# Kernel tuning notes

Measured on AMD Instinct MI355X. Metric: run time of the kernel, lower is better.

The kernel has to match this reference:

```python
import jax, jax.numpy as jnp
import numpy as np

B, T, H, S, NH = 8, 4096, 1024, 64, 16
DH = H // NH
L = T // S  # tokens per sentence (contiguous partition)


def setup_inputs() -> dict:
    key = jax.random.key(0)
    ks = jax.random.split(key, 10)
    init = lambda k, shape: (jax.random.normal(k, shape, dtype=jnp.float32) * 0.02)
    starts = jnp.arange(S, dtype=jnp.int32) * L
    bounds = jnp.stack([starts, starts + L], axis=-1)  # [S,2]
    sentence_boundaries = jnp.broadcast_to(bounds, (B, S, 2))
    return {
        "context_hidden": jax.random.normal(ks[0], (B, T, H), dtype=jnp.float32),
        "sentence_boundaries": sentence_boundaries,
        "in_proj_w": init(ks[1], (3 * H, H)),
        "in_proj_b": jnp.zeros((3 * H,), jnp.float32),
        "out_w": init(ks[2], (H, H)),
        "out_b": jnp.zeros((H,), jnp.float32),
        "w1": init(ks[3], (H, 2 * H)),
        "b1": jnp.zeros((H,), jnp.float32),
        "w2": init(ks[4], (1, H)),
        "b2": jnp.zeros((1,), jnp.float32),
    }


def _forward(h, sentence_boundaries, in_proj_w, in_proj_b, out_w, out_b, w1, b1, w2, b2):
    starts = sentence_boundaries[:, :, 0]  # [B,S]
    ends = sentence_boundaries[:, :, 1]    # [B,S]
    t = jnp.arange(T, dtype=jnp.int32)
    # membership: token t belongs to sentence s iff start <= t < end
    member = (t[None, :, None] >= starts[:, None, :]) & (t[None, :, None] < ends[:, None, :])  # [B,T,S]
    mf = member.astype(h.dtype)
    counts = jnp.clip(mf.sum(axis=1), 1.0)  # [B,S]
    # segment mean pooling (encode_sentences)
    sent_repr = jnp.einsum('bts,bth->bsh', mf, h) / counts[..., None]  # [B,S,H]

    # multihead self-attention over sentence reprs (eval mode, no dropout)
    qkv = sent_repr @ in_proj_w.T + in_proj_b  # [B,S,3H]
    q, k, v = jnp.split(qkv, 3, axis=-1)
    q = q.reshape(B, S, NH, DH)
    k = k.reshape(B, S, NH, DH)
    v = v.reshape(B, S, NH, DH)
    scores = jnp.einsum('bqhd,bkhd->bhqk', q, k) / jnp.sqrt(jnp.asarray(DH, h.dtype))
    attn = jax.nn.softmax(scores, axis=-1)
    ctx = jnp.einsum('bhqk,bkhd->bqhd', attn, v).reshape(B, S, H)
    attended = ctx @ out_w.T + out_b  # [B,S,H]

    # gather each token's sentence repr
    sid = jnp.clip(member.astype(jnp.int32).argmax(axis=-1), 0, S - 1)  # [B,T]
    covered = member.any(axis=-1)  # [B,T]
    att_tok = jnp.take_along_axis(attended, sid[..., None], axis=1)  # [B,T,H]

    # coherence scorer MLP on concat([token, sent_repr]) without materializing concat
    hid = jax.nn.relu(h @ w1[:, :H].T + att_tok @ w1[:, H:].T + b1)  # [B,T,H]
    score = (hid @ w2.T + b2)[..., 0]  # [B,T]
    score = jnp.where(covered, score, 0.0)
    return h + score[..., None] * h


def reference(context_hidden, sentence_boundaries, in_proj_w, in_proj_b, out_w, out_b, w1, b1, w2, b2):
    return _forward(context_hidden, sentence_boundaries, in_proj_w, in_proj_b,
                    out_w, out_b, w1, b1, w2, b2)
```

## Files before the change

kernel.cpp:

```cpp
#include <hip/hip_runtime.h>
#include <stdint.h>

#define BB 8
#define TT 4096
#define HH 1024
#define SS 64
#define NHH 16
#define DHH 64

typedef __attribute__((ext_vector_type(8))) short short8;
typedef __attribute__((ext_vector_type(8))) unsigned short ushortx8;
typedef __attribute__((ext_vector_type(4))) float f32x4;
typedef unsigned short u16;

#define GLOAD16(gp, lp)                                                   \
  __builtin_amdgcn_global_load_lds(                                      \
      (const __attribute__((address_space(1))) void*)(gp),               \
      (__attribute__((address_space(3))) void*)(lp), 16, 0, 0)

__device__ __forceinline__ u16 f2bf(float f) {
  union { float f; uint32_t u; } v;
  v.f = f;
  uint32_t u = v.u;
  uint32_t r = u + 0x7fffu + ((u >> 16) & 1u);
  return (u16)(r >> 16);
}

__device__ __forceinline__ float bf2f(u16 b) {
  union { uint32_t u; float f; } v;
  v.u = ((uint32_t)b) << 16;
  return v.f;
}

__device__ __forceinline__ void stage_tile(u16* lds, const float* src, int ld, int tid) {
#pragma unroll
  for (int q = 0; q < 4; ++q) {
    int slot_id = tid + (q << 8);
    int row = slot_id >> 3;
    int sl = slot_id & 7;
    const float* p = src + (size_t)row * ld + (sl << 3);
    float4 x0 = *(const float4*)(p);
    float4 x1 = *(const float4*)(p + 4);
    ushortx8 o;
    o[0] = f2bf(x0.x); o[1] = f2bf(x0.y); o[2] = f2bf(x0.z); o[3] = f2bf(x0.w);
    o[4] = f2bf(x1.x); o[5] = f2bf(x1.y); o[6] = f2bf(x1.z); o[7] = f2bf(x1.w);
    *(ushortx8*)(&lds[(row << 6) + (((sl ^ (row & 7)) << 3))]) = o;
  }
}

__global__ __launch_bounds__(256) void conv_tile_kernel(const float* __restrict__ src,
                                                        int ld, int ntile_k,
                                                        u16* __restrict__ dst) {
  int bid = blockIdx.x;
  int rt = bid / ntile_k;
  int kt = bid - rt * ntile_k;
  const float* s0 = src + (size_t)rt * 128 * ld + kt * 64;
  u16* d0 = dst + (size_t)bid * 8192;
  int tid = threadIdx.x;
#pragma unroll
  for (int q = 0; q < 4; ++q) {
    int slot_id = tid + (q << 8);
    int row = slot_id >> 3;
    int sl = slot_id & 7;
    const float* p = s0 + (size_t)row * ld + (sl << 3);
    float4 x0 = *(const float4*)(p);
    float4 x1 = *(const float4*)(p + 4);
    ushortx8 o;
    o[0] = f2bf(x0.x); o[1] = f2bf(x0.y); o[2] = f2bf(x0.z); o[3] = f2bf(x0.w);
    o[4] = f2bf(x1.x); o[5] = f2bf(x1.y); o[6] = f2bf(x1.z); o[7] = f2bf(x1.w);
    *(ushortx8*)(&d0[(row << 6) + (((sl ^ (row & 7)) << 3))]) = o;
  }
}

__global__ __launch_bounds__(256) void pool_bf_kernel(const u16* __restrict__ hbf,
                                                      const int* __restrict__ bounds,
                                                      float* __restrict__ sent) {
  int bs = blockIdx.x;
  int b = bs >> 6;
  int start = bounds[bs * 2];
  int end = bounds[bs * 2 + 1];
  int lo = max(start, 0), hi = min(end, TT);
  int cnt = max(hi - lo, 0);
  float inv = 1.0f / (float)max(cnt, 1);
  int tid = threadIdx.x;
  int sg = tid >> 1;
  int half = tid & 1;
  int kt = sg >> 3, slot = sg & 7;
  float a[8] = {};
  for (int t = lo + half; t < hi; t += 2) {
    int grow = b * TT + t;
    int rt = grow >> 7, r = grow & 127;
    const u16* tile = hbf + ((size_t)rt * 16 + kt) * 8192;
    ushortx8 v = *(const ushortx8*)(&tile[(r << 6) + ((slot ^ (r & 7)) << 3)]);
#pragma unroll
    for (int j = 0; j < 8; ++j) a[j] += bf2f(v[j]);
  }
#pragma unroll
  for (int j = 0; j < 8; ++j) a[j] += __shfl_xor(a[j], 1);
  if (half == 0) {
    float* d = sent + (size_t)bs * HH + sg * 8;
#pragma unroll
    for (int j = 0; j < 8; ++j) d[j] = a[j] * inv;
  }
}

__global__ __launch_bounds__(256) void setup_misc(const float* __restrict__ ipb,
                                                  const float* __restrict__ outb,
                                                  const float* __restrict__ b1,
                                                  const int* __restrict__ bounds,
                                                  float* __restrict__ qkv,
                                                  float* __restrict__ att,
                                                  float* __restrict__ cbuf,
                                                  int* __restrict__ sid) {
  int idx = blockIdx.x * 256 + threadIdx.x;
  const int STR = 2048 * 256;
  for (int i = idx; i < 512 * 3072; i += STR) qkv[i] = ipb[i % 3072];
  for (int i = idx; i < 512 * 1024; i += STR) att[i] = outb[i & 1023];
  for (int i = idx; i < 512 * 1024; i += STR) cbuf[i] = b1[i & 1023];
  if (idx < BB * TT) {
    int b = idx >> 12, t = idx & (TT - 1);
    int r = -1;
    for (int s = 0; s < SS; ++s) {
      int st = bounds[(b * SS + s) * 2], en = bounds[(b * SS + s) * 2 + 1];
      if (t >= st && t < en) { r = s; break; }
    }
    sid[idx] = r;
  }
}

__global__ __launch_bounds__(256) void gemm_bt_atomic(const float* __restrict__ A, int lda,
                                                      const float* __restrict__ Bm, int ldb,
                                                      float* __restrict__ C, int ldc,
                                                      int kper) {
  __shared__ u16 As[128 * 64];
  __shared__ u16 Bs[128 * 64];
  int tid = threadIdx.x;
  int m0 = blockIdx.x * 128, n0 = blockIdx.y * 128;
  int kbeg = blockIdx.z * kper;
  f32x4 acc[4][4] = {};

  for (int k0 = kbeg; k0 < kbeg + kper; k0 += 64) {
    __syncthreads();
    stage_tile(As, A + (size_t)m0 * lda + k0, lda, tid);
    stage_tile(Bs, Bm + (size_t)n0 * ldb + k0, ldb, tid);
    __syncthreads();
    int lane = tid & 63, wid = tid >> 6;
    int wm = wid >> 1, wn = wid & 1;
    int lr = lane & 15, lg = lane >> 4;
#pragma unroll
    for (int kk = 0; kk < 2; ++kk) {
      short8 af[4], bfr[4];
#pragma unroll
      for (int i = 0; i < 4; ++i) {
        int arow = wm * 64 + i * 16 + lr;
        int aslot = (kk * 4 + lg) ^ (arow & 7);
        af[i] = *(const short8*)(&As[(arow << 6) + (aslot << 3)]);
        int brow = wn * 64 + i * 16 + lr;
        int bslot = (kk * 4 + lg) ^ (brow & 7);
        bfr[i] = *(const short8*)(&Bs[(brow << 6) + (bslot << 3)]);
      }
#pragma unroll
      for (int i = 0; i < 4; ++i)
#pragma unroll
        for (int j = 0; j < 4; ++j)
          acc[i][j] = __builtin_amdgcn_mfma_f32_16x16x32_bf16(af[i], bfr[j], acc[i][j], 0, 0, 0);
    }
  }

  int lane = tid & 63, wid = tid >> 6;
  int wm = wid >> 1, wn = wid & 1;
  int lr = lane & 15, lg = lane >> 4;
#pragma unroll
  for (int i = 0; i < 4; ++i)
#pragma unroll
    for (int j = 0; j < 4; ++j)
#pragma unroll
      for (int r = 0; r < 4; ++r) {
        int row = m0 + wm * 64 + i * 16 + lg * 4 + r;
        int col = n0 + wn * 64 + j * 16 + lr;
        atomicAdd(&C[(size_t)row * ldc + col], acc[i][j][r]);
      }
}

__global__ __launch_bounds__(256) void attn_kernel(const float* __restrict__ qkv,
                                                   float* __restrict__ ctx) {
  int bh = blockIdx.x;
  int b = bh >> 4, nh = bh & 15;
  __shared__ float q[64][64], k[64][64], v[64][64], s[64][64];
  int tid = threadIdx.x;
  const float* base = qkv + (size_t)b * SS * 3072 + nh * 64;
  for (int e = tid; e < 4096; e += 256) {
    int i = e >> 6, d = e & 63;
    q[i][d] = base[(size_t)i * 3072 + d];
    k[i][d] = base[(size_t)i * 3072 + 1024 + d];
    v[i][d] = base[(size_t)i * 3072 + 2048 + d];
  }
  __syncthreads();
  for (int e = tid; e < 4096; e += 256) {
    int i = e >> 6, j = e & 63;
    float acc = 0.f;
#pragma unroll 8
    for (int d = 0; d < 64; ++d) acc += q[i][d] * k[j][d];
    s[i][j] = acc * 0.125f;
  }
  __syncthreads();
  {
    int r = tid >> 2, sub = tid & 3;
    int j0 = sub * 16;
    float m = -1e30f;
#pragma unroll
    for (int j = 0; j < 16; ++j) m = fmaxf(m, s[r][j0 + j]);
    m = fmaxf(m, __shfl_xor(m, 1));
    m = fmaxf(m, __shfl_xor(m, 2));
    float sum = 0.f;
#pragma unroll
    for (int j = 0; j < 16; ++j) {
      float e_ = __expf(s[r][j0 + j] - m);
      s[r][j0 + j] = e_;
      sum += e_;
    }
    sum += __shfl_xor(sum, 1);
    sum += __shfl_xor(sum, 2);
    float inv = 1.0f / sum;
#pragma unroll
    for (int j = 0; j < 16; ++j) s[r][j0 + j] *= inv;
  }
  __syncthreads();
  for (int e = tid; e < 4096; e += 256) {
    int i = e >> 6, d = e & 63;
    float acc = 0.f;
#pragma unroll 8
    for (int j = 0; j < 64; ++j) acc += s[i][j] * v[j][d];
    ctx[((size_t)b * SS + i) * HH + nh * 64 + d] = acc;
  }
}

__global__ __launch_bounds__(512, 4) void score_partial(const u16* __restrict__ hbf,
                                                        const u16* __restrict__ wbf,
                                                        const float* __restrict__ cbuf,
                                                        const float* __restrict__ w2,
                                                        const int* __restrict__ sid_arr,
                                                        float* __restrict__ score_part) {
  __shared__ u16 As[8192];
  __shared__ u16 Bs[16384];
  __shared__ float w2_lds[256];
  __shared__ int sid_lds[128];
  __shared__ float red[128];

  int tid = threadIdx.x;
  int bid = blockIdx.x;
  int x = bid & 7;
  int g = bid >> 3;
  int mt = x * 32 + (g >> 2);
  int c = g & 3;
  int n0 = c * 256;
  size_t g0 = (size_t)mt * 128;
  int b = (int)(g0 >> 12);
  const u16* asrc = hbf + (size_t)mt * 16 * 8192;

  if (tid < 256) w2_lds[tid] = w2[n0 + tid];
  if (tid < 128) {
    sid_lds[tid] = sid_arr[g0 + tid];
    red[tid] = 0.f;
  }

  int lane = tid & 63, wid = tid >> 6;
  int wm = wid >> 2, wn = wid & 3;
  int lr = lane & 15, lg = lane >> 4;

  f32x4 acc[4][4] = {};
  for (int kt = 0; kt < 16; ++kt) {
    __syncthreads();
    const u16* at = asrc + kt * 8192;
#pragma unroll
    for (int q = 0; q < 2; ++q) {
      int off = q * 4096 + wid * 512;
      GLOAD16(at + off + lane * 8, &As[off]);
    }
#pragma unroll
    for (int q = 0; q < 4; ++q) {
      int half = q >> 1;
      int boff = (q & 1) * 4096 + wid * 512;
      const u16* bt = wbf + ((size_t)(2 * c + half) * 16 + kt) * 8192;
      GLOAD16(bt + boff + lane * 8, &Bs[half * 8192 + boff]);
    }
    __syncthreads();
#pragma unroll
    for (int kk = 0; kk < 2; ++kk) {
      short8 af[4], bfr[4];
#pragma unroll
      for (int i = 0; i < 4; ++i) {
        int arow = wm * 64 + i * 16 + lr;
        int aslot = (kk * 4 + lg) ^ (arow & 7);
        af[i] = *(const short8*)(&As[(arow << 6) + (aslot << 3)]);
      }
#pragma unroll
      for (int j = 0; j < 4; ++j) {
        int brow = wn * 64 + j * 16 + lr;
        int half = (wn * 64 + j * 16) >> 7;
        int r = brow & 127;
        int bslot = (kk * 4 + lg) ^ (r & 7);
        bfr[j] = *(const short8*)(&Bs[(half << 13) + (r << 6) + (bslot << 3)]);
      }
#pragma unroll
      for (int i = 0; i < 4; ++i)
#pragma unroll
        for (int j = 0; j < 4; ++j)
          acc[i][j] = __builtin_amdgcn_mfma_f32_16x16x32_bf16(af[i], bfr[j], acc[i][j], 0, 0, 0);
    }
  }

  float sp[4][4];
#pragma unroll
  for (int i = 0; i < 4; ++i) {
#pragma unroll
    for (int r = 0; r < 4; ++r) {
      int rowl = wm * 64 + i * 16 + lg * 4 + r;
      int s = sid_lds[rowl];
      int sc = s < 0 ? 0 : s;
      const float* crow = cbuf + ((size_t)b * SS + sc) * HH + n0;
      float accs = 0.f;
#pragma unroll
      for (int j = 0; j < 4; ++j) {
        int coll = wn * 64 + j * 16 + lr;
        float t = acc[i][j][r] + crow[coll];
        if (t > 0.f) accs += t * w2_lds[coll];
      }
      sp[i][r] = accs;
    }
  }

#pragma unroll
  for (int i = 0; i < 4; ++i)
#pragma unroll
    for (int r = 0; r < 4; ++r) {
      float v = sp[i][r];
      v += __shfl_xor(v, 1);
      v += __shfl_xor(v, 2);
      v += __shfl_xor(v, 4);
      v += __shfl_xor(v, 8);
      sp[i][r] = v;
    }
  if (lr == 0) {
#pragma unroll
    for (int i = 0; i < 4; ++i)
#pragma unroll
      for (int r = 0; r < 4; ++r)
        atomicAdd(&red[wm * 64 + i * 16 + lg * 4 + r], sp[i][r]);
  }
  __syncthreads();
  if (tid < 128) score_part[(size_t)c * (BB * TT) + g0 + tid] = red[tid];
}

__global__ __launch_bounds__(256) void scale_kernel(const u16* __restrict__ hbf,
                                                    const float* __restrict__ score_part,
                                                    const float* __restrict__ b2,
                                                    const int* __restrict__ sid_arr,
                                                    float* __restrict__ out) {
  __shared__ float fac[16];
  int tid = threadIdx.x;
  int r0 = blockIdx.x * 16;
  if (tid < 16) {
    int t = r0 + tid;
    float s = b2[0];
#pragma unroll
    for (int c = 0; c < 4; ++c) s += score_part[(size_t)c * (BB * TT) + t];
    fac[tid] = (sid_arr[t] >= 0) ? (1.0f + s) : 1.0f;
  }
  __syncthreads();
  for (int e = tid; e < 16 * 128; e += 256) {
    int row = e >> 7, grp = e & 127;
    int kt = grp >> 3, slot = grp & 7;
    int grow = r0 + row;
    int rt = grow >> 7, r = grow & 127;
    const u16* tile = hbf + ((size_t)rt * 16 + kt) * 8192;
    ushortx8 v = *(const ushortx8*)(&tile[(r << 6) + ((slot ^ (r & 7)) << 3)]);
    float f = fac[row];
    float4 o0, o1;
    o0.x = bf2f(v[0]) * f; o0.y = bf2f(v[1]) * f; o0.z = bf2f(v[2]) * f; o0.w = bf2f(v[3]) * f;
    o1.x = bf2f(v[4]) * f; o1.y = bf2f(v[5]) * f; o1.z = bf2f(v[6]) * f; o1.w = bf2f(v[7]) * f;
    float4* dst = (float4*)(out + (size_t)grow * HH + grp * 8);
    dst[0] = o0;
    dst[1] = o1;
  }
}

extern "C" void kernel_launch(void* const* d_in, const int* in_sizes, int n_in,
                              void* d_out, int out_size, void* d_ws, size_t ws_size,
                              hipStream_t stream) {
  const float* h        = (const float*)d_in[0];
  const int*   bounds   = (const int*)d_in[1];
  const float* in_proj_w = (const float*)d_in[2];
  const float* in_proj_b = (const float*)d_in[3];
  const float* out_w    = (const float*)d_in[4];
  const float* out_b    = (const float*)d_in[5];
  const float* w1       = (const float*)d_in[6];
  const float* b1       = (const float*)d_in[7];
  const float* w2       = (const float*)d_in[8];
  const float* b2       = (const float*)d_in[9];
  float* out = (float*)d_out;

  char* ws = (char*)d_ws;
  float* sent  = (float*)(ws);
  float* qkv   = (float*)(ws + (2ull << 20));
  float* ctx   = (float*)(ws + (8ull << 20));
  float* att   = (float*)(ws + (10ull << 20));
  float* cbuf  = (float*)(ws + (12ull << 20));
  int*   sid   = (int*)(ws + (14ull << 20));
  float* spart = (float*)(ws + (15ull << 20));
  u16*   hbf   = (u16*)(ws + (16ull << 20));
  u16*   wbf   = (u16*)(ws + (80ull << 20));

  conv_tile_kernel<<<256 * 16, 256, 0, stream>>>(h, HH, 16, hbf);
  conv_tile_kernel<<<8 * 16, 256, 0, stream>>>(w1, 2 * HH, 16, wbf);

  pool_bf_kernel<<<BB * SS, 256, 0, stream>>>(hbf, bounds, sent);
  setup_misc<<<2048, 256, 0, stream>>>(in_proj_b, out_b, b1, bounds, qkv, att, cbuf, sid);

  gemm_bt_atomic<<<dim3(4, 24, 4), 256, 0, stream>>>(sent, HH, in_proj_w, HH, qkv, 3 * HH, 256);
  attn_kernel<<<BB * NHH, 256, 0, stream>>>(qkv, ctx);
  gemm_bt_atomic<<<dim3(4, 8, 4), 256, 0, stream>>>(ctx, HH, out_w, HH, att, HH, 256);
  gemm_bt_atomic<<<dim3(4, 8, 4), 256, 0, stream>>>(att, HH, w1 + HH, 2 * HH, cbuf, HH, 256);

  score_partial<<<1024, 512, 0, stream>>>(hbf, wbf, cbuf, w2, sid, spart);
  scale_kernel<<<2048, 256, 0, stream>>>(hbf, spart, b2, sid, out);
}
```

Baseline: 288.7 us.

## Enlarge score GEMM tile to 256x256 with 1024-thread blocks; merge conversion launches

The token-scoring GEMM now uses 256x256 output tiles per block (16 waves, 1024 threads) instead of 128x256. Each loaded weight tile is reused across twice as many token rows, which cuts global/L2 traffic for W1 per output. The two fp32-to-bf16 conversion launches are also merged into one kernel to save a launch. The larger block halves the grid to 512 blocks and raises LDS use and per-CU register pressure, which may lower occupancy and latency hiding.

```diff
diff --git a/kernel.cpp b/kernel.cpp
--- a/kernel.cpp
+++ b/kernel.cpp
@@ -48,14 +48,19 @@
   }
 }
 
-__global__ __launch_bounds__(256) void conv_tile_kernel(const float* __restrict__ src,
-                                                        int ld, int ntile_k,
-                                                        u16* __restrict__ dst) {
+__global__ __launch_bounds__(256) void conv_both_kernel(const float* __restrict__ h,
+                                                        u16* __restrict__ hbf,
+                                                        const float* __restrict__ w1,
+                                                        u16* __restrict__ wbf) {
   int bid = blockIdx.x;
-  int rt = bid / ntile_k;
-  int kt = bid - rt * ntile_k;
+  const float* src;
+  int ld, tbid;
+  u16* dst;
+  if (bid < 4096) { src = h;  ld = 1024; dst = hbf; tbid = bid; }
+  else            { src = w1; ld = 2048; dst = wbf; tbid = bid - 4096; }
+  int rt = tbid >> 4, kt = tbid & 15;
   const float* s0 = src + (size_t)rt * 128 * ld + kt * 64;
-  u16* d0 = dst + (size_t)bid * 8192;
+  u16* d0 = dst + (size_t)tbid * 8192;
   int tid = threadIdx.x;
 #pragma unroll
   for (int q = 0; q < 4; ++q) {
@@ -235,54 +240,51 @@
   }
 }
 
-__global__ __launch_bounds__(512, 4) void score_partial(const u16* __restrict__ hbf,
-                                                        const u16* __restrict__ wbf,
-                                                        const float* __restrict__ cbuf,
-                                                        const float* __restrict__ w2,
-                                                        const int* __restrict__ sid_arr,
-                                                        float* __restrict__ score_part) {
-  __shared__ u16 As[8192];
-  __shared__ u16 Bs[16384];
+__global__ __launch_bounds__(1024, 4) void score_partial(const u16* __restrict__ hbf,
+                                                         const u16* __restrict__ wbf,
+                                                         const float* __restrict__ cbuf,
+                                                         const float* __restrict__ w2,
+                                                         const int* __restrict__ sid_arr,
+                                                         float* __restrict__ score_part) {
+  __shared__ u16 As[2][8192];
+  __shared__ u16 Bs[2][8192];
   __shared__ float w2_lds[256];
-  __shared__ int sid_lds[128];
-  __shared__ float red[128];
+  __shared__ int sid_lds[256];
+  __shared__ float red[256];
 
   int tid = threadIdx.x;
   int bid = blockIdx.x;
   int x = bid & 7;
   int g = bid >> 3;
-  int mt = x * 32 + (g >> 2);
+  int mt = x * 16 + (g >> 2);
   int c = g & 3;
   int n0 = c * 256;
-  size_t g0 = (size_t)mt * 128;
+  size_t g0 = (size_t)mt * 256;
   int b = (int)(g0 >> 12);
-  const u16* asrc = hbf + (size_t)mt * 16 * 8192;
-
-  if (tid < 256) w2_lds[tid] = w2[n0 + tid];
-  if (tid < 128) {
+  const u16* a0 = hbf + (size_t)(2 * mt) * 16 * 8192;
+  const u16* a1 = hbf + (size_t)(2 * mt + 1) * 16 * 8192;
+  const u16* b0 = wbf + (size_t)(2 * c) * 16 * 8192;
+  const u16* b1 = wbf + (size_t)(2 * c + 1) * 16 * 8192;
+
+  if (tid < 256) {
+    w2_lds[tid] = w2[n0 + tid];
     sid_lds[tid] = sid_arr[g0 + tid];
     red[tid] = 0.f;
   }
 
   int lane = tid & 63, wid = tid >> 6;
-  int wm = wid >> 2, wn = wid & 3;
+  int wr = wid >> 2, wc = wid & 3;
   int lr = lane & 15, lg = lane >> 4;
 
   f32x4 acc[4][4] = {};
   for (int kt = 0; kt < 16; ++kt) {
     __syncthreads();
-    const u16* at = asrc + kt * 8192;
-#pragma unroll
-    for (int q = 0; q < 2; ++q) {
-      int off = q * 4096 + wid * 512;
-      GLOAD16(at + off + lane * 8, &As[off]);
-    }
-#pragma unroll
-    for (int q = 0; q < 4; ++q) {
-      int half = q >> 1;
-      int boff = (q & 1) * 4096 + wid * 512;
-      const u16* bt = wbf + ((size_t)(2 * c + half) * 16 + kt) * 8192;
-      GLOAD16(bt + boff + lane * 8, &Bs[half * 8192 + boff]);
+    {
+      int off = wid * 512;
+      GLOAD16(a0 + (size_t)kt * 8192 + off + lane * 8, &As[0][off]);
+      GLOAD16(a1 + (size_t)kt * 8192 + off + lane * 8, &As[1][off]);
+      GLOAD16(b0 + (size_t)kt * 8192 + off + lane * 8, &Bs[0][off]);
+      GLOAD16(b1 + (size_t)kt * 8192 + off + lane * 8, &Bs[1][off]);
     }
     __syncthreads();
 #pragma unroll
@@ -290,17 +292,17 @@
       short8 af[4], bfr[4];
 #pragma unroll
       for (int i = 0; i < 4; ++i) {
-        int arow = wm * 64 + i * 16 + lr;
-        int aslot = (kk * 4 + lg) ^ (arow & 7);
-        af[i] = *(const short8*)(&As[(arow << 6) + (aslot << 3)]);
+        int arow = wr * 64 + i * 16 + lr;
+        int ah = arow >> 7, r = arow & 127;
+        int aslot = (kk * 4 + lg) ^ (r & 7);
+        af[i] = *(const short8*)(&As[ah][(r << 6) + (aslot << 3)]);
       }
 #pragma unroll
       for (int j = 0; j < 4; ++j) {
-        int brow = wn * 64 + j * 16 + lr;
-        int half = (wn * 64 + j * 16) >> 7;
-        int r = brow & 127;
+        int brow = wc * 64 + j * 16 + lr;
+        int bh = brow >> 7, r = brow & 127;
         int bslot = (kk * 4 + lg) ^ (r & 7);
-        bfr[j] = *(const short8*)(&Bs[(half << 13) + (r << 6) + (bslot << 3)]);
+        bfr[j] = *(const short8*)(&Bs[bh][(r << 6) + (bslot << 3)]);
       }
 #pragma unroll
       for (int i = 0; i < 4; ++i)
@@ -315,14 +317,14 @@
   for (int i = 0; i < 4; ++i) {
 #pragma unroll
     for (int r = 0; r < 4; ++r) {
-      int rowl = wm * 64 + i * 16 + lg * 4 + r;
+      int rowl = wr * 64 + i * 16 + lg * 4 + r;
       int s = sid_lds[rowl];
       int sc = s < 0 ? 0 : s;
       const float* crow = cbuf + ((size_t)b * SS + sc) * HH + n0;
       float accs = 0.f;
 #pragma unroll
       for (int j = 0; j < 4; ++j) {
-        int coll = wn * 64 + j * 16 + lr;
+        int coll = wc * 64 + j * 16 + lr;
         float t = acc[i][j][r] + crow[coll];
         if (t > 0.f) accs += t * w2_lds[coll];
       }
@@ -346,10 +348,10 @@
     for (int i = 0; i < 4; ++i)
 #pragma unroll
       for (int r = 0; r < 4; ++r)
-        atomicAdd(&red[wm * 64 + i * 16 + lg * 4 + r], sp[i][r]);
+        atomicAdd(&red[wr * 64 + i * 16 + lg * 4 + r], sp[i][r]);
   }
   __syncthreads();
-  if (tid < 128) score_part[(size_t)c * (BB * TT) + g0 + tid] = red[tid];
+  if (tid < 256) score_part[(size_t)c * (BB * TT) + g0 + tid] = red[tid];
 }
 
 __global__ __launch_bounds__(256) void scale_kernel(const u16* __restrict__ hbf,
@@ -411,8 +413,7 @@
   u16*   hbf   = (u16*)(ws + (16ull << 20));
   u16*   wbf   = (u16*)(ws + (80ull << 20));
 
-  conv_tile_kernel<<<256 * 16, 256, 0, stream>>>(h, HH, 16, hbf);
-  conv_tile_kernel<<<8 * 16, 256, 0, stream>>>(w1, 2 * HH, 16, wbf);
+  conv_both_kernel<<<4096 + 128, 256, 0, stream>>>(h, hbf, w1, wbf);
 
   pool_bf_kernel<<<BB * SS, 256, 0, stream>>>(hbf, bounds, sent);
   setup_misc<<<2048, 256, 0, stream>>>(in_proj_b, out_b, b1, bounds, qkv, att, cbuf, sid);
@@ -422,6 +423,6 @@
   gemm_bt_atomic<<<dim3(4, 8, 4), 256, 0, stream>>>(ctx, HH, out_w, HH, att, HH, 256);
   gemm_bt_atomic<<<dim3(4, 8, 4), 256, 0, stream>>>(att, HH, w1 + HH, 2 * HH, cbuf, HH, 256);
 
-  score_partial<<<1024, 512, 0, stream>>>(hbf, wbf, cbuf, w2, sid, spart);
+  score_partial<<<512, 1024, 0, stream>>>(hbf, wbf, cbuf, w2, sid, spart);
   scale_kernel<<<2048, 256, 0, stream>>>(hbf, spart, b2, sid, out);
 }
```

Result: slower. 296.0 us (+2.5%).
